# Performance work log

Measured on AMD Instinct MI355X. Metric: run time of the kernel, lower is better.

## Reference

```python
import jax, jax.numpy as jnp
import numpy as np

N_SRC = 50000   # nodes of src type
N_TRG = 50000   # nodes of trg type
H = 256         # hidden_size
E = 300000      # number of labeled edges for this message type


def setup_inputs() -> dict:
    key = jax.random.key(0)
    k0, k1, k2, k3 = jax.random.split(key, 4)
    x_src = jax.random.normal(k0, (N_SRC, H), dtype=jnp.float32)
    x_trg = jax.random.normal(k1, (N_TRG, H), dtype=jnp.float32)
    # nn.Parameter(torch.rand(H, H) * 0.01)
    R = jax.random.uniform(k2, (H, H), dtype=jnp.float32) * 0.01
    edge_index = jax.random.randint(k3, (2, E), 0, N_SRC, dtype=jnp.int64)
    return {"x_src": x_src, "x_trg": x_trg, "R": R, "edge_index": edge_index}


def reference(x_src, x_trg, R, edge_index):
    # Gather per-edge endpoint embeddings (index_select on dim 0).
    nodes_left = x_src[edge_index[0]]    # (E, H)
    nodes_right = x_trg[edge_index[1]]   # (E, H)
    # Original: sum((nodes_right @ R) @ nodes_left.T, dim=-1)
    # == (nodes_right @ R) @ nodes_left.sum(0)  -- same math, avoids the E x E
    # intermediate which is infeasible to materialize at this scale.
    left_sum = nodes_left.sum(axis=0)    # (H,)
    scores = (nodes_right @ R) @ left_sum  # (E,)
    return scores
```

## Files before the change

### kernel.cpp

```cpp
#include <hip/hip_runtime.h>

#define HDIM 256
#define NBLK 1024

__global__ void k_zero(uint4* __restrict__ p, int n4) {
    int i = blockIdx.x * blockDim.x + threadIdx.x;
    if (i < n4) p[i] = make_uint4(0u, 0u, 0u, 0u);
}

__global__ void k_count(const int* __restrict__ src, int E, unsigned int* __restrict__ counts) {
    int e = blockIdx.x * blockDim.x + threadIdx.x;
    if (e < E) atomicAdd(&counts[src[e]], 1u);
}

__global__ void k_colsum_partial(const float4* __restrict__ x4,
                                 const unsigned int* __restrict__ counts,
                                 int N, float* __restrict__ partials) {
    int colgrp = threadIdx.x & 63;
    int rowOff = threadIdx.x >> 6;
    float4 acc = make_float4(0.f, 0.f, 0.f, 0.f);
    for (int n = blockIdx.x * 4 + rowOff; n < N; n += NBLK * 4) {
        float c = (float)counts[n];
        float4 x = x4[(size_t)n * 64 + colgrp];
        acc.x += c * x.x; acc.y += c * x.y; acc.z += c * x.z; acc.w += c * x.w;
    }
    __shared__ float s[4 * HDIM];
    int col = colgrp * 4;
    s[rowOff * HDIM + col + 0] = acc.x;
    s[rowOff * HDIM + col + 1] = acc.y;
    s[rowOff * HDIM + col + 2] = acc.z;
    s[rowOff * HDIM + col + 3] = acc.w;
    __syncthreads();
    int tid = threadIdx.x;
    partials[(size_t)blockIdx.x * HDIM + tid] =
        s[tid] + s[HDIM + tid] + s[2 * HDIM + tid] + s[3 * HDIM + tid];
}

__global__ __launch_bounds__(1024)
void k_reduce_matvec(const float* __restrict__ partials,
                     const float* __restrict__ Rm,
                     float* __restrict__ v) {
    __shared__ float red[4][HDIM];
    __shared__ float lss[HDIM];
    const int tid = threadIdx.x;
    const int h = tid & (HDIM - 1);
    const int q = tid >> 8;

    const float* p = partials + (size_t)q * (NBLK / 4) * HDIM + h;
    float acc = 0.f;
    #pragma unroll 16
    for (int b = 0; b < NBLK / 4; ++b) acc += p[(size_t)b * HDIM];
    red[q][h] = acc;
    __syncthreads();
    if (q == 0) lss[h] = red[0][h] + red[1][h] + red[2][h] + red[3][h];
    __syncthreads();

    const float4* R4 = (const float4*)(Rm + (size_t)h * HDIM);
    float a = 0.f;
    #pragma unroll
    for (int j = q * 16; j < q * 16 + 16; ++j) {
        float4 r = R4[j];
        a += r.x * lss[4 * j] + r.y * lss[4 * j + 1] + r.z * lss[4 * j + 2] + r.w * lss[4 * j + 3];
    }
    red[q][h] = a;
    __syncthreads();
    if (q == 0) v[h] = red[0][h] + red[1][h] + red[2][h] + red[3][h];
}

__global__ void k_rowdot(const float4* __restrict__ x4, const float* __restrict__ v,
                         int N, float* __restrict__ t) {
    __shared__ float4 vs[64];
    int tid = threadIdx.x;
    if (tid < 64) vs[tid] = ((const float4*)v)[tid];
    __syncthreads();
    int lane = tid & 63;
    int wid = tid >> 6;
    int n = blockIdx.x * 4 + wid;
    if (n < N) {
        float4 x = x4[(size_t)n * 64 + lane];
        float4 vv = vs[lane];
        float d = x.x * vv.x + x.y * vv.y + x.z * vv.z + x.w * vv.w;
        #pragma unroll
        for (int off = 32; off > 0; off >>= 1) d += __shfl_down(d, off, 64);
        if (lane == 0) t[n] = d;
    }
}

__global__ void k_gather(const int* __restrict__ trg, int E, const float* __restrict__ t,
                         float* __restrict__ out) {
    int e = blockIdx.x * blockDim.x + threadIdx.x;
    if (e < E) out[e] = t[trg[e]];
}

extern "C" void kernel_launch(void* const* d_in, const int* in_sizes, int n_in,
                              void* d_out, int out_size, void* d_ws, size_t ws_size,
                              hipStream_t stream) {
    const float* x_src = (const float*)d_in[0];
    const float* x_trg = (const float*)d_in[1];
    const float* Rm    = (const float*)d_in[2];
    const int*   edge  = (const int*)d_in[3];
    float* out = (float*)d_out;

    const int N_src = in_sizes[0] / HDIM;
    const int N_trg = in_sizes[1] / HDIM;
    const int E     = in_sizes[3] / 2;

    char* ws = (char*)d_ws;
    size_t off = 0;
    auto alloc = [&](size_t bytes) -> void* {
        void* p = ws + off;
        off = (off + bytes + 255) & ~(size_t)255;
        return p;
    };
    unsigned int* counts = (unsigned int*)alloc((size_t)N_src * sizeof(unsigned int));
    float* partials      = (float*)alloc((size_t)NBLK * HDIM * sizeof(float));
    float* v             = (float*)alloc(HDIM * sizeof(float));
    float* t             = (float*)alloc((size_t)N_trg * sizeof(float));
    (void)ws_size; (void)n_in; (void)out_size;

    const int n4 = (N_src + 3) / 4;
    k_zero<<<(n4 + 255) / 256, 256, 0, stream>>>((uint4*)counts, n4);

    k_count<<<(E + 255) / 256, 256, 0, stream>>>(edge, E, counts);
    k_colsum_partial<<<NBLK, 256, 0, stream>>>((const float4*)x_src, counts, N_src, partials);
    k_reduce_matvec<<<1, 1024, 0, stream>>>(partials, Rm, v);
    k_rowdot<<<(N_trg + 3) / 4, 256, 0, stream>>>((const float4*)x_trg, v, N_trg, t);
    k_gather<<<(E + 255) / 256, 256, 0, stream>>>(edge + E, E, t, out);
}
```

Before: 65.94 us.

## Fuse column-sum reduction and matvec via fixed-point atomics and last-block ticket

```diff
diff --git a/kernel.cpp b/kernel.cpp
--- a/kernel.cpp
+++ b/kernel.cpp
@@ -2,25 +2,44 @@
 
 #define HDIM 256
 #define NBLK 1024
+#define NREP 8
+#define FXSCALE 16777216.0f
+#define FXINV   5.9604644775390625e-8f
 
 __global__ void k_zero(uint4* __restrict__ p, int n4) {
     int i = blockIdx.x * blockDim.x + threadIdx.x;
     if (i < n4) p[i] = make_uint4(0u, 0u, 0u, 0u);
 }
 
-__global__ void k_count(const int* __restrict__ src, int E, unsigned int* __restrict__ counts) {
-    int e = blockIdx.x * blockDim.x + threadIdx.x;
-    if (e < E) atomicAdd(&counts[src[e]], 1u);
+__global__ void k_count(const int4* __restrict__ src4, const int* __restrict__ src,
+                        int E, int N, unsigned int* __restrict__ counts8) {
+    int i = blockIdx.x * blockDim.x + threadIdx.x;
+    unsigned int* c = counts8 + (size_t)(blockIdx.x & (NREP - 1)) * N;
+    int E4 = E >> 2;
+    if (i < E4) {
+        int4 v = src4[i];
+        atomicAdd(&c[v.x], 1u); atomicAdd(&c[v.y], 1u);
+        atomicAdd(&c[v.z], 1u); atomicAdd(&c[v.w], 1u);
+    }
+    if (i < (E & 3)) {
+        atomicAdd(&counts8[src[(E4 << 2) + i]], 1u);
+    }
 }
 
-__global__ void k_colsum_partial(const float4* __restrict__ x4,
-                                 const unsigned int* __restrict__ counts,
-                                 int N, float* __restrict__ partials) {
-    int colgrp = threadIdx.x & 63;
-    int rowOff = threadIdx.x >> 6;
+__global__ __launch_bounds__(256)
+void k_colsum_matvec(const float4* __restrict__ x4,
+                     const unsigned int* __restrict__ counts8, int N,
+                     const float* __restrict__ Rm,
+                     unsigned long long* __restrict__ acc64,
+                     unsigned int* __restrict__ ticket,
+                     float* __restrict__ v) {
+    const int colgrp = threadIdx.x & 63;
+    const int rowOff = threadIdx.x >> 6;
     float4 acc = make_float4(0.f, 0.f, 0.f, 0.f);
     for (int n = blockIdx.x * 4 + rowOff; n < N; n += NBLK * 4) {
-        float c = (float)counts[n];
+        float c = 0.f;
+        #pragma unroll
+        for (int r = 0; r < NREP; ++r) c += (float)counts8[(size_t)r * N + n];
         float4 x = x4[(size_t)n * 64 + colgrp];
         acc.x += c * x.x; acc.y += c * x.y; acc.z += c * x.z; acc.w += c * x.w;
     }
@@ -31,40 +50,30 @@
     s[rowOff * HDIM + col + 2] = acc.z;
     s[rowOff * HDIM + col + 3] = acc.w;
     __syncthreads();
-    int tid = threadIdx.x;
-    partials[(size_t)blockIdx.x * HDIM + tid] =
-        s[tid] + s[HDIM + tid] + s[2 * HDIM + tid] + s[3 * HDIM + tid];
-}
-
-__global__ __launch_bounds__(1024)
-void k_reduce_matvec(const float* __restrict__ partials,
-                     const float* __restrict__ Rm,
-                     float* __restrict__ v) {
-    __shared__ float red[4][HDIM];
-    __shared__ float lss[HDIM];
     const int tid = threadIdx.x;
-    const int h = tid & (HDIM - 1);
-    const int q = tid >> 8;
-
-    const float* p = partials + (size_t)q * (NBLK / 4) * HDIM + h;
-    float acc = 0.f;
-    #pragma unroll 16
-    for (int b = 0; b < NBLK / 4; ++b) acc += p[(size_t)b * HDIM];
-    red[q][h] = acc;
+    float part = s[tid] + s[HDIM + tid] + s[2 * HDIM + tid] + s[3 * HDIM + tid];
+    long long q = (long long)llrintf(part * FXSCALE);
+    atomicAdd(&acc64[tid], (unsigned long long)q);
+    __threadfence();
     __syncthreads();
-    if (q == 0) lss[h] = red[0][h] + red[1][h] + red[2][h] + red[3][h];
+    __shared__ unsigned int lastflag;
+    if (tid == 0) lastflag = (atomicAdd(ticket, 1u) == NBLK - 1) ? 1u : 0u;
     __syncthreads();
-
-    const float4* R4 = (const float4*)(Rm + (size_t)h * HDIM);
-    float a = 0.f;
-    #pragma unroll
-    for (int j = q * 16; j < q * 16 + 16; ++j) {
-        float4 r = R4[j];
-        a += r.x * lss[4 * j] + r.y * lss[4 * j + 1] + r.z * lss[4 * j + 2] + r.w * lss[4 * j + 3];
+    if (lastflag) {
+        __threadfence();
+        __shared__ float lss[HDIM];
+        long long qv = (long long)atomicAdd(&acc64[tid], 0ull);
+        lss[tid] = (float)qv * FXINV;
+        __syncthreads();
+        const float4* R4 = (const float4*)(Rm + (size_t)tid * HDIM);
+        float a = 0.f;
+        #pragma unroll
+        for (int j = 0; j < 64; ++j) {
+            float4 r = R4[j];
+            a += r.x * lss[4 * j] + r.y * lss[4 * j + 1] + r.z * lss[4 * j + 2] + r.w * lss[4 * j + 3];
+        }
+        v[tid] = a;
     }
-    red[q][h] = a;
-    __syncthreads();
-    if (q == 0) v[h] = red[0][h] + red[1][h] + red[2][h] + red[3][h];
 }
 
 __global__ void k_rowdot(const float4* __restrict__ x4, const float* __restrict__ v,
@@ -86,10 +95,19 @@
     }
 }
 
-__global__ void k_gather(const int* __restrict__ trg, int E, const float* __restrict__ t,
-                         float* __restrict__ out) {
-    int e = blockIdx.x * blockDim.x + threadIdx.x;
-    if (e < E) out[e] = t[trg[e]];
+__global__ void k_gather(const int4* __restrict__ trg4, const int* __restrict__ trg, int E,
+                         const float* __restrict__ t,
+                         float4* __restrict__ out4, float* __restrict__ out) {
+    int i = blockIdx.x * blockDim.x + threadIdx.x;
+    int E4 = E >> 2;
+    if (i < E4) {
+        int4 v = trg4[i];
+        out4[i] = make_float4(t[v.x], t[v.y], t[v.z], t[v.w]);
+    }
+    if (i < (E & 3)) {
+        int e = (E4 << 2) + i;
+        out[e] = t[trg[e]];
+    }
 }
 
 extern "C" void kernel_launch(void* const* d_in, const int* in_sizes, int n_in,
@@ -112,18 +130,29 @@
         off = (off + bytes + 255) & ~(size_t)255;
         return p;
     };
-    unsigned int* counts = (unsigned int*)alloc((size_t)N_src * sizeof(unsigned int));
-    float* partials      = (float*)alloc((size_t)NBLK * HDIM * sizeof(float));
-    float* v             = (float*)alloc(HDIM * sizeof(float));
-    float* t             = (float*)alloc((size_t)N_trg * sizeof(float));
+    const size_t counts_bytes = (size_t)NREP * N_src * sizeof(unsigned int);
+    const size_t zbytes = counts_bytes + HDIM * sizeof(unsigned long long) + 256;
+    unsigned int* zbase = (unsigned int*)alloc(zbytes);
+    unsigned int* counts8 = zbase;
+    unsigned long long* acc64 = (unsigned long long*)((char*)zbase + counts_bytes);
+    unsigned int* ticket = (unsigned int*)(acc64 + HDIM);
+    float* v = (float*)alloc(HDIM * sizeof(float));
+    float* t = (float*)alloc((size_t)N_trg * sizeof(float));
     (void)ws_size; (void)n_in; (void)out_size;
 
-    const int n4 = (N_src + 3) / 4;
-    k_zero<<<(n4 + 255) / 256, 256, 0, stream>>>((uint4*)counts, n4);
+    const int n4 = (int)(zbytes / 16);
+    k_zero<<<(n4 + 255) / 256, 256, 0, stream>>>((uint4*)zbase, n4);
 
-    k_count<<<(E + 255) / 256, 256, 0, stream>>>(edge, E, counts);
-    k_colsum_partial<<<NBLK, 256, 0, stream>>>((const float4*)x_src, counts, N_src, partials);
-    k_reduce_matvec<<<1, 1024, 0, stream>>>(partials, Rm, v);
+    const int E4 = E >> 2;
+    const int cntThreads = (E4 > 0 ? E4 : 1);
+    k_count<<<(cntThreads + 255) / 256, 256, 0, stream>>>(
+        (const int4*)edge, edge, E, N_src, counts8);
+
+    k_colsum_matvec<<<NBLK, 256, 0, stream>>>(
+        (const float4*)x_src, counts8, N_src, Rm, acc64, ticket, v);
+
     k_rowdot<<<(N_trg + 3) / 4, 256, 0, stream>>>((const float4*)x_trg, v, N_trg, t);
-    k_gather<<<(E + 255) / 256, 256, 0, stream>>>(edge + E, E, t, out);
+
+    k_gather<<<(cntThreads + 255) / 256, 256, 0, stream>>>(
+        (const int4*)(edge + E), edge + E, E, t, (float4*)out, out);
 }
```

Measured after the change: 124.7 us. 1.89x slower.
